# Optimization experiments

Hardware: AMD Instinct MI355X
Metric: run time of the kernel (lower is better)

Reference implementation:

```python
import jax, jax.numpy as jnp
import numpy as np
import math

N_EMBD = 1024
N_HEAD = 16
HEAD_DIM = N_EMBD // N_HEAD


def setup_inputs() -> dict:
    key = jax.random.key(0)
    k_x, k_w1, k_b1, k_w2, k_b2 = jax.random.split(key, 5)
    B, T = 2, 2048
    x = jax.random.normal(k_x, (B, T, N_EMBD), dtype=jnp.float32)
    # ln1: Linear(n_embd, 3*n_embd); weights stored as [in, out] for x @ W
    W_qkv = jax.random.normal(k_w1, (N_EMBD, 3 * N_EMBD), dtype=jnp.float32) * 0.02
    b_qkv = jax.random.normal(k_b1, (3 * N_EMBD,), dtype=jnp.float32) * 0.02
    # ln2: Linear(n_embd, n_embd)
    W_out = jax.random.normal(k_w2, (N_EMBD, N_EMBD), dtype=jnp.float32) * 0.02
    b_out = jax.random.normal(k_b2, (N_EMBD,), dtype=jnp.float32) * 0.02
    return {"x": x, "W_qkv": W_qkv, "b_qkv": b_qkv, "W_out": W_out, "b_out": b_out}


def reference(x, W_qkv, b_qkv, W_out, b_out):
    B, T, C = x.shape
    qkv = x @ W_qkv + b_qkv                      # [B,T,3C]
    q, k, v = jnp.split(qkv, 3, axis=-1)
    # reshape to heads: [B, H, T, D]
    def to_heads(t):
        return t.reshape(B, T, N_HEAD, HEAD_DIM).transpose(0, 2, 1, 3)
    Q, K, V = to_heads(q), to_heads(k), to_heads(v)
    # NOTE: scale is 1/sqrt(n_head), as in the source (not sqrt(head_dim));
    # NOTE: no causal mask is applied, faithfully matching the source forward.
    scale = 1.0 / math.sqrt(N_HEAD)
    scores = jnp.einsum('bhqd,bhkd->bhqk', Q, K) * scale  # [B,H,T,T]
    attn = jax.nn.softmax(scores, axis=-1)
    out = jnp.einsum('bhqk,bhkd->bhqd', attn, V)          # [B,H,T,D]
    out = out.transpose(0, 2, 1, 3).reshape(B, T, C)
    # dropout = 0.0 -> identity (eval mode)
    return out @ W_out + b_out
```

## Files before the change

kernel.cpp:

```cpp
#include <hip/hip_runtime.h>
#include <hip/hip_bf16.h>
#include <stdint.h>

typedef __bf16 bf16_t;
typedef __bf16 bf16x8 __attribute__((ext_vector_type(8)));
typedef float  f32x4  __attribute__((ext_vector_type(4)));

#define AS1 __attribute__((address_space(1)))
#define AS3 __attribute__((address_space(3)))

__device__ __forceinline__ void gload16(const bf16_t* g, char* l) {
  __builtin_amdgcn_global_load_lds((AS1 const void*)(uintptr_t)g, (AS3 void*)l, 16, 0, 0);
}
__device__ __forceinline__ int swz8(int r) { return (r & 7) ^ ((r >> 2) & 6); }

#define C2S 0.36067376022224085f
#define LGKM0 do { asm volatile("s_waitcnt lgkmcnt(0)" ::: "memory"); \
                   __builtin_amdgcn_sched_barrier(0); } while (0)

__global__ __launch_bounds__(256) void prep(
    const float* __restrict__ x, const float* __restrict__ Wqkv, const float* __restrict__ Wout,
    bf16_t* __restrict__ xb, bf16_t* __restrict__ wqkvT, bf16_t* __restrict__ woutT) {
  __shared__ float tile[32][33];
  const int bid = blockIdx.x, tid = threadIdx.x;
  if (bid < 4096) {
    const int i = bid * 256 + tid;
    float4 v = reinterpret_cast<const float4*>(x)[i];
    union { bf16_t h[4]; unsigned long long u; } r;
    r.h[0] = (bf16_t)v.x; r.h[1] = (bf16_t)v.y; r.h[2] = (bf16_t)v.z; r.h[3] = (bf16_t)v.w;
    reinterpret_cast<unsigned long long*>(xb)[i] = r.u;
    return;
  }
  const float* W; bf16_t* Wt; int N, tb;
  if (bid < 7168) { W = Wqkv; Wt = wqkvT; N = 3072; tb = bid - 4096; }
  else            { W = Wout; Wt = woutT; N = 1024; tb = bid - 7168; }
  const int kb = (tb & 31) * 32, nb = (tb >> 5) * 32;
  const int tx = tid & 31, ty = tid >> 5;
#pragma unroll
  for (int i = 0; i < 32; i += 8)
    tile[ty + i][tx] = W[(size_t)(kb + ty + i) * N + nb + tx];
  __syncthreads();
#pragma unroll
  for (int i = 0; i < 32; i += 8)
    Wt[(size_t)(nb + ty + i) * 1024 + kb + tx] = (bf16_t)tile[tx][ty + i];
}

template<int MI>
__global__ __launch_bounds__(256) void gemm_bt(
    const bf16_t* __restrict__ A, const bf16_t* __restrict__ Bt,
    const float* __restrict__ bias,
    bf16_t* __restrict__ outb, bf16_t* __restrict__ vtb, float* __restrict__ outf,
    int M, int N, int K, int ldo, int mode) {
  __shared__ bf16_t lA[3][MI * 1024];
  __shared__ bf16_t lB[3][4096];
  const int tid = threadIdx.x;
  const int wave = tid >> 6, lane = tid & 63;
  const int lr = lane & 15, lg = lane >> 4;
  const int ntiles = N >> 7;
  const int bid = (blockIdx.x & 7) * ((int)gridDim.x >> 3) + (blockIdx.x >> 3);
  const int bn = bid % ntiles, bm = bid / ntiles;
  const int m0 = bm * (MI * 32), n0 = bn * 128;
  const int wr = wave >> 1, wc = wave & 1;
  f32x4 acc[MI][4] = {};

  const int lamw = wave * 64 + lane;
  const int srow = lamw >> 2;
  const int scolb = ((lamw & 3) << 4) ^ (((srow >> 1) & 3) << 4);
  auto stageA = [&](int buf, int k0, int it) {
    gload16(A + (size_t)(m0 + it * 64 + srow) * K + k0 + (scolb >> 1),
            (char*)&lA[buf][0] + (it * 256 + wave * 64) * 16);
  };
  auto stageB = [&](int buf, int k0, int it) {
    gload16(Bt + (size_t)(n0 + it * 64 + srow) * K + k0 + (scolb >> 1),
            (char*)&lB[buf][0] + (it * 256 + wave * 64) * 16);
  };
  auto stageg = [&](int buf, int k0) {
#pragma unroll
    for (int it = 0; it < MI / 2; ++it) stageA(buf, k0, it);
    stageB(buf, k0, 0); stageB(buf, k0, 1);
  };

  auto ldA = [&](const char* p, int mi) {
    const int row = wr * (MI * 16) + mi * 16 + lr;
    return *reinterpret_cast<const bf16x8*>(p + row * 64 + ((lg * 16) ^ (((row >> 1) & 3) << 4)));
  };
  auto ldB = [&](const char* p, int ni) {
    const int row = wc * 64 + ni * 16 + lr;
    return *reinterpret_cast<const bf16x8*>(p + row * 64 + ((lg * 16) ^ (((row >> 1) & 3) << 4)));
  };

  const int nt = K >> 5;
  stageg(0, 0);
  stageg(1, 32);
  int cur = 0, stg = 2;

  for (int t = 0; t < nt; ++t) {
    if (t + 1 < nt) {
      if constexpr (MI == 4) asm volatile("s_waitcnt vmcnt(4)" ::: "memory");
      else                   asm volatile("s_waitcnt vmcnt(3)" ::: "memory");
    } else {
      asm volatile("s_waitcnt vmcnt(0)" ::: "memory");
    }
    __builtin_amdgcn_s_barrier();
    __builtin_amdgcn_sched_barrier(0);

    const char* pA = (const char*)&lA[cur][0];
    const char* pB = (const char*)&lB[cur][0];
    const bool pf = (t + 2 < nt);
    const int k2 = (t + 2) << 5;
    bf16x8 af[MI], bfv[4];

    if constexpr (MI == 4) {
      af[0] = ldA(pA, 0); af[1] = ldA(pA, 1);
      bfv[0] = ldB(pB, 0); bfv[1] = ldB(pB, 1);
      if (pf) stageA(stg, k2, 0);
      __builtin_amdgcn_s_barrier(); LGKM0;
      __builtin_amdgcn_s_setprio(1);
      acc[0][0] = __builtin_amdgcn_mfma_f32_16x16x32_bf16(af[0], bfv[0], acc[0][0], 0, 0, 0);
      acc[0][1] = __builtin_amdgcn_mfma_f32_16x16x32_bf16(af[0], bfv[1], acc[0][1], 0, 0, 0);
      acc[1][0] = __builtin_amdgcn_mfma_f32_16x16x32_bf16(af[1], bfv[0], acc[1][0], 0, 0, 0);
      acc[1][1] = __builtin_amdgcn_mfma_f32_16x16x32_bf16(af[1], bfv[1], acc[1][1], 0, 0, 0);
      __builtin_amdgcn_s_setprio(0);
      bfv[2] = ldB(pB, 2); bfv[3] = ldB(pB, 3);
      if (pf) stageA(stg, k2, 1);
      __builtin_amdgcn_s_barrier(); LGKM0;
      __builtin_amdgcn_s_setprio(1);
      acc[0][2] = __builtin_amdgcn_mfma_f32_16x16x32_bf16(af[0], bfv[2], acc[0][2], 0, 0, 0);
      acc[0][3] = __builtin_amdgcn_mfma_f32_16x16x32_bf16(af[0], bfv[3], acc[0][3], 0, 0, 0);
      acc[1][2] = __builtin_amdgcn_mfma_f32_16x16x32_bf16(af[1], bfv[2], acc[1][2], 0, 0, 0);
      acc[1][3] = __builtin_amdgcn_mfma_f32_16x16x32_bf16(af[1], bfv[3], acc[1][3], 0, 0, 0);
      __builtin_amdgcn_s_setprio(0);
      af[2] = ldA(pA, 2); af[3] = ldA(pA, 3);
      if (pf) stageB(stg, k2, 0);
      __builtin_amdgcn_s_barrier(); LGKM0;
      __builtin_amdgcn_s_setprio(1);
      acc[2][0] = __builtin_amdgcn_mfma_f32_16x16x32_bf16(af[2], bfv[0], acc[2][0], 0, 0, 0);
      acc[2][1] = __builtin_amdgcn_mfma_f32_16x16x32_bf16(af[2], bfv[1], acc[2][1], 0, 0, 0);
      acc[3][0] = __builtin_amdgcn_mfma_f32_16x16x32_bf16(af[3], bfv[0], acc[3][0], 0, 0, 0);
      acc[3][1] = __builtin_amdgcn_mfma_f32_16x16x32_bf16(af[3], bfv[1], acc[3][1], 0, 0, 0);
      __builtin_amdgcn_s_setprio(0);
      if (pf) stageB(stg, k2, 1);
      __builtin_amdgcn_s_barrier();
      __builtin_amdgcn_s_setprio(1);
      acc[2][2] = __builtin_amdgcn_mfma_f32_16x16x32_bf16(af[2], bfv[2], acc[2][2], 0, 0, 0);
      acc[2][3] = __builtin_amdgcn_mfma_f32_16x16x32_bf16(af[2], bfv[3], acc[2][3], 0, 0, 0);
      acc[3][2] = __builtin_amdgcn_mfma_f32_16x16x32_bf16(af[3], bfv[2], acc[3][2], 0, 0, 0);
      acc[3][3] = __builtin_amdgcn_mfma_f32_16x16x32_bf16(af[3], bfv[3], acc[3][3], 0, 0, 0);
      __builtin_amdgcn_s_setprio(0);
    } else {
      af[0] = ldA(pA, 0); af[1] = ldA(pA, 1);
      bfv[0] = ldB(pB, 0); bfv[1] = ldB(pB, 1);
      if (pf) { stageA(stg, k2, 0); stageB(stg, k2, 0); }
      __builtin_amdgcn_s_barrier(); LGKM0;
      __builtin_amdgcn_s_setprio(1);
      acc[0][0] = __builtin_amdgcn_mfma_f32_16x16x32_bf16(af[0], bfv[0], acc[0][0], 0, 0, 0);
      acc[0][1] = __builtin_amdgcn_mfma_f32_16x16x32_bf16(af[0], bfv[1], acc[0][1], 0, 0, 0);
      acc[1][0] = __builtin_amdgcn_mfma_f32_16x16x32_bf16(af[1], bfv[0], acc[1][0], 0, 0, 0);
      acc[1][1] = __builtin_amdgcn_mfma_f32_16x16x32_bf16(af[1], bfv[1], acc[1][1], 0, 0, 0);
      __builtin_amdgcn_s_setprio(0);
      bfv[2] = ldB(pB, 2); bfv[3] = ldB(pB, 3);
      if (pf) stageB(stg, k2, 1);
      __builtin_amdgcn_s_barrier(); LGKM0;
      __builtin_amdgcn_s_setprio(1);
      acc[0][2] = __builtin_amdgcn_mfma_f32_16x16x32_bf16(af[0], bfv[2], acc[0][2], 0, 0, 0);
      acc[0][3] = __builtin_amdgcn_mfma_f32_16x16x32_bf16(af[0], bfv[3], acc[0][3], 0, 0, 0);
      acc[1][2] = __builtin_amdgcn_mfma_f32_16x16x32_bf16(af[1], bfv[2], acc[1][2], 0, 0, 0);
      acc[1][3] = __builtin_amdgcn_mfma_f32_16x16x32_bf16(af[1], bfv[3], acc[1][3], 0, 0, 0);
      __builtin_amdgcn_s_setprio(0);
    }

    cur = cur == 2 ? 0 : cur + 1;
    stg = stg == 2 ? 0 : stg + 1;
  }

#pragma unroll
  for (int mi = 0; mi < MI; ++mi) {
#pragma unroll
    for (int ni = 0; ni < 4; ++ni) {
      const int col = n0 + wc * 64 + ni * 16 + lr;
      const float bv = bias[col];
      const int rg0 = m0 + wr * (MI * 16) + mi * 16 + lg * 4;
      if (mode == 1 && col >= 2048) {
        const int colv = col - 2048;
        const int dd = colv & 63, hh = colv >> 6;
        const int bb = rg0 >> 11, t = rg0 & 2047;
        union { bf16_t h4[4]; unsigned long long u; } pk;
#pragma unroll
        for (int r = 0; r < 4; ++r) pk.h4[r] = (bf16_t)(acc[mi][ni][r] + bv);
        *reinterpret_cast<unsigned long long*>(
            vtb + (size_t)(bb * 16 + hh) * 131072 + (size_t)dd * 2048 + t) = pk.u;
      } else {
        const float sc = (mode == 1 && col < 1024) ? C2S : 1.f;
#pragma unroll
        for (int r = 0; r < 4; ++r) {
          const float v = (acc[mi][ni][r] + bv) * sc;
          if (mode == 2) outf[(size_t)(rg0 + r) * ldo + col] = v;
          else           outb[(size_t)(rg0 + r) * ldo + col] = (bf16_t)v;
        }
      }
    }
  }
}

__global__ __launch_bounds__(512) void attn_fwd(
    const bf16_t* __restrict__ qkv2,
    const bf16_t* __restrict__ vT,
    bf16_t* __restrict__ a0, bf16_t* __restrict__ a1,
    float* __restrict__ lbuf) {
  __shared__ bf16_t lds[3][8192];
  const int tid = threadIdx.x;
  const int wave = tid >> 6, lane = tid & 63;
  const int lr = lane & 15, lg = lane >> 4;
  const int id = blockIdx.x;
  const int xcd = id & 7, slot = id >> 3;
  const int bh = xcd * 4 + (slot & 3);
  const int rest = slot >> 2;
  const int qb = rest & 7, kvh = rest >> 3;
  const int b = bh >> 4, h = bh & 15;

  const int q0 = qb * 256 + wave * 32;
  const bf16_t* Qp = qkv2 + (size_t)(b * 2048 + q0) * 2048 + h * 64;
  bf16x8 qf[2][2];
#pragma unroll
  for (int hx = 0; hx < 2; ++hx) {
    qf[hx][0] = *reinterpret_cast<const bf16x8*>(Qp + (size_t)(hx * 16 + lr) * 2048 + lg * 8);
    qf[hx][1] = *reinterpret_cast<const bf16x8*>(Qp + (size_t)(hx * 16 + lr) * 2048 + 32 + lg * 8);
  }

  const int kr = tid >> 3;
  const int ks = (tid & 7) ^ swz8(kr);
  const bf16_t* Ksrc = qkv2 + (size_t)(b * 2048 + kvh * 1024 + kr) * 2048 + 1024 + h * 64 + ks * 8;
  const bf16_t* Vsrc = vT + (size_t)bh * 131072 + (size_t)kr * 2048 + kvh * 1024 + ks * 8;

  auto stage = [&](int buf, int kb) {
    char* base = (char*)&lds[buf][0] + wave * 1024;
    gload16(Ksrc + (size_t)kb * 131072, base);
    gload16(Vsrc + (size_t)kb * 64, base + 8192);
  };

  int kofs[4][2], vofs[4][2];
#pragma unroll
  for (int t = 0; t < 4; ++t) {
    const int kk = 32 * (t >> 1) + 8 * (lr >> 2) + 4 * (t & 1) + (lr & 3);
    const int sw = swz8(kk) << 4;
    kofs[t][0] = (kk << 7) + ((lg * 16) ^ sw);
    kofs[t][1] = (kk << 7) + ((64 + lg * 16) ^ sw);
  }
#pragma unroll
  for (int nc = 0; nc < 4; ++nc) {
    const int vr = nc * 16 + lr;
    const int sw = swz8(vr) << 4;
    vofs[nc][0] = 8192 + (vr << 7) + ((lg * 16) ^ sw);
    vofs[nc][1] = 8192 + (vr << 7) + ((64 + lg * 16) ^ sw);
  }

  f32x4 acc[2][4] = {};
  f32x4 accl[2] = {};
  bf16x8 ones;
#pragma unroll
  for (int j = 0; j < 8; ++j) ones[j] = (bf16_t)1.0f;

  stage(0, 0);
  stage(1, 1);
  int cur = 0, stg = 2;

  for (int kb = 0; kb < 16; ++kb) {
    if (kb + 2 < 16) stage(stg, kb + 2);
    if (kb + 2 < 16)      asm volatile("s_waitcnt vmcnt(4)" ::: "memory");
    else if (kb + 1 < 16) asm volatile("s_waitcnt vmcnt(2)" ::: "memory");
    else                  asm volatile("s_waitcnt vmcnt(0)" ::: "memory");
    __builtin_amdgcn_s_barrier();
    __builtin_amdgcn_sched_barrier(0);
    const char* bK = (const char*)&lds[cur][0];

    f32x4 s[2][4];
#pragma unroll
    for (int t = 0; t < 4; ++t) {
      const bf16x8 k0 = *reinterpret_cast<const bf16x8*>(bK + kofs[t][0]);
      const bf16x8 k1 = *reinterpret_cast<const bf16x8*>(bK + kofs[t][1]);
#pragma unroll
      for (int hx = 0; hx < 2; ++hx) {
        f32x4 z = {0.f, 0.f, 0.f, 0.f};
        z = __builtin_amdgcn_mfma_f32_16x16x32_bf16(k0, qf[hx][0], z, 0, 0, 0);
        s[hx][t] = __builtin_amdgcn_mfma_f32_16x16x32_bf16(k1, qf[hx][1], z, 0, 0, 0);
      }
    }

    bf16x8 pa[2][2];
#pragma unroll
    for (int hx = 0; hx < 2; ++hx) {
      float p[16];
#pragma unroll
      for (int t = 0; t < 4; ++t)
#pragma unroll
        for (int r = 0; r < 4; ++r)
          p[t * 4 + r] = __builtin_amdgcn_exp2f(s[hx][t][r]);
#pragma unroll
      for (int j = 0; j < 8; ++j) { pa[hx][0][j] = (bf16_t)p[j]; pa[hx][1][j] = (bf16_t)p[8 + j]; }
    }

    __builtin_amdgcn_s_setprio(1);
#pragma unroll
    for (int hx = 0; hx < 2; ++hx) {
      accl[hx] = __builtin_amdgcn_mfma_f32_16x16x32_bf16(pa[hx][0], ones, accl[hx], 0, 0, 0);
      accl[hx] = __builtin_amdgcn_mfma_f32_16x16x32_bf16(pa[hx][1], ones, accl[hx], 0, 0, 0);
    }
#pragma unroll
    for (int nc = 0; nc < 4; ++nc) {
      const bf16x8 v0 = *reinterpret_cast<const bf16x8*>(bK + vofs[nc][0]);
      const bf16x8 v1 = *reinterpret_cast<const bf16x8*>(bK + vofs[nc][1]);
#pragma unroll
      for (int hx = 0; hx < 2; ++hx) {
        acc[hx][nc] = __builtin_amdgcn_mfma_f32_16x16x32_bf16(pa[hx][0], v0, acc[hx][nc], 0, 0, 0);
        acc[hx][nc] = __builtin_amdgcn_mfma_f32_16x16x32_bf16(pa[hx][1], v1, acc[hx][nc], 0, 0, 0);
      }
    }
    __builtin_amdgcn_s_setprio(0);

    __builtin_amdgcn_sched_barrier(0);
    __builtin_amdgcn_s_barrier();
    cur = cur == 2 ? 0 : cur + 1;
    stg = stg == 2 ? 0 : stg + 1;
  }

  bf16_t* ap = kvh ? a1 : a0;
#pragma unroll
  for (int hx = 0; hx < 2; ++hx) {
#pragma unroll
    for (int r = 0; r < 4; ++r) {
      const float lf = 1.f / accl[hx][r];
      const int qg = q0 + hx * 16 + lg * 4 + r;
      bf16_t* op = ap + (size_t)(b * 2048 + qg) * 1024 + h * 64 + lr;
#pragma unroll
      for (int nc = 0; nc < 4; ++nc) op[nc * 16] = (bf16_t)(acc[hx][nc][r] * lf);
      if (lr == 0)
        lbuf[(size_t)(kvh * 4096 + b * 2048 + qg) * 16 + h] = accl[hx][r];
    }
  }
}

__global__ void attn_reduce(const bf16_t* __restrict__ a0, const bf16_t* __restrict__ a1,
                            const float* __restrict__ lbuf, bf16_t* __restrict__ aout) {
  const int i = blockIdx.x * 256 + threadIdx.x;
  const int r = i >> 7, h = (i & 127) >> 3;
  const float l0 = lbuf[(size_t)r * 16 + h];
  const float l1 = lbuf[(size_t)(4096 + r) * 16 + h];
  const float inv = 1.f / (l0 + l1);
  const float w0 = l0 * inv, w1 = l1 * inv;
  const bf16x8 v0 = reinterpret_cast<const bf16x8*>(a0)[i];
  const bf16x8 v1 = reinterpret_cast<const bf16x8*>(a1)[i];
  bf16x8 o;
#pragma unroll
  for (int j = 0; j < 8; ++j) o[j] = (bf16_t)(w0 * (float)v0[j] + w1 * (float)v1[j]);
  reinterpret_cast<bf16x8*>(aout)[i] = o;
}

extern "C" void kernel_launch(void* const* d_in, const int* in_sizes, int n_in,
                              void* d_out, int out_size, void* d_ws, size_t ws_size,
                              hipStream_t stream) {
  (void)in_sizes; (void)n_in; (void)out_size; (void)ws_size;
  const float* x    = (const float*)d_in[0];
  const float* Wqkv = (const float*)d_in[1];
  const float* bqkv = (const float*)d_in[2];
  const float* Wout = (const float*)d_in[3];
  const float* bout = (const float*)d_in[4];
  float* out = (float*)d_out;

  char* ws = (char*)d_ws;
  bf16_t* xb    = (bf16_t*)(ws);
  bf16_t* a0    = (bf16_t*)(ws);
  bf16_t* wqkvT = (bf16_t*)(ws + 8388608);
  bf16_t* woutT = (bf16_t*)(ws + 14680064);
  bf16_t* qkv2  = (bf16_t*)(ws + 16777216);
  bf16_t* aout  = (bf16_t*)(ws + 16777216);
  bf16_t* vT    = (bf16_t*)(ws + 33554432);
  bf16_t* a1    = (bf16_t*)(ws + 41943040);
  float*  lbuf  = (float*)(ws + 50331648);

  prep<<<8192, 256, 0, stream>>>(x, Wqkv, Wout, xb, wqkvT, woutT);
  gemm_bt<4><<<768, 256, 0, stream>>>(xb, wqkvT, bqkv, qkv2, vT, nullptr, 4096, 3072, 1024, 2048, 1);
  attn_fwd<<<512, 512, 0, stream>>>(qkv2, vT, a0, a1, lbuf);
  attn_reduce<<<2048, 256, 0, stream>>>(a0, a1, lbuf, aout);
  gemm_bt<2><<<512, 256, 0, stream>>>(aout, woutT, bout, nullptr, nullptr, out, 4096, 1024, 1024, 1024, 2);
}
```

Baseline: 114.2 us.

## Use 8-wave 128x128 GEMM kernel for QKV projection with simpler pipeline

```diff
diff --git a/kernel.cpp b/kernel.cpp
--- a/kernel.cpp
+++ b/kernel.cpp
@@ -43,6 +43,109 @@
 #pragma unroll
   for (int i = 0; i < 32; i += 8)
     Wt[(size_t)(nb + ty + i) * 1024 + kb + tx] = (bf16_t)tile[tx][ty + i];
+}
+
+__global__ __launch_bounds__(512) void gemm8(
+    const bf16_t* __restrict__ A, const bf16_t* __restrict__ Bt,
+    const float* __restrict__ bias,
+    bf16_t* __restrict__ outb, bf16_t* __restrict__ vtb,
+    int N, int K, int ldo) {
+  __shared__ bf16_t lA[3][4096];
+  __shared__ bf16_t lB[3][4096];
+  const int tid = threadIdx.x;
+  const int wave = tid >> 6, lane = tid & 63;
+  const int lr = lane & 15, lg = lane >> 4;
+  const int ntiles = N >> 7;
+  const int bid = (blockIdx.x & 7) * ((int)gridDim.x >> 3) + (blockIdx.x >> 3);
+  const int bn = bid % ntiles, bm = bid / ntiles;
+  const int m0 = bm * 128, n0 = bn * 128;
+  const int wr = wave >> 2, wc = wave & 3;
+  f32x4 acc[4][2] = {};
+
+  const int srow = tid >> 2;
+  const int scolb = ((tid & 3) << 4) ^ (((srow >> 1) & 3) << 4);
+  const bf16_t* Asrc = A  + (size_t)(m0 + srow) * K + (scolb >> 1);
+  const bf16_t* Bsrc = Bt + (size_t)(n0 + srow) * K + (scolb >> 1);
+  auto stage = [&](int buf, int k0) {
+    char* dst = (char*)nullptr;
+    (void)dst;
+    gload16(Asrc + k0, (char*)&lA[buf][0] + wave * 1024);
+    gload16(Bsrc + k0, (char*)&lB[buf][0] + wave * 1024);
+  };
+
+  auto ldA = [&](const char* p, int mi) {
+    const int row = wr * 64 + mi * 16 + lr;
+    return *reinterpret_cast<const bf16x8*>(p + row * 64 + ((lg * 16) ^ (((row >> 1) & 3) << 4)));
+  };
+  auto ldB = [&](const char* p, int ni) {
+    const int row = wc * 32 + ni * 16 + lr;
+    return *reinterpret_cast<const bf16x8*>(p + row * 64 + ((lg * 16) ^ (((row >> 1) & 3) << 4)));
+  };
+
+  const int nt = K >> 5;
+  stage(0, 0);
+  stage(1, 32);
+  int cur = 0, stg = 2;
+
+  for (int t = 0; t < nt; ++t) {
+    if (t + 2 < nt) {
+      stage(stg, (t + 2) << 5);
+      asm volatile("s_waitcnt vmcnt(4)" ::: "memory");
+    } else if (t + 1 < nt) {
+      asm volatile("s_waitcnt vmcnt(2)" ::: "memory");
+    } else {
+      asm volatile("s_waitcnt vmcnt(0)" ::: "memory");
+    }
+    __builtin_amdgcn_s_barrier();
+    __builtin_amdgcn_sched_barrier(0);
+
+    const char* pA = (const char*)&lA[cur][0];
+    const char* pB = (const char*)&lB[cur][0];
+    bf16x8 af[4], bfv[2];
+#pragma unroll
+    for (int mi = 0; mi < 4; ++mi) af[mi] = ldA(pA, mi);
+    bfv[0] = ldB(pB, 0); bfv[1] = ldB(pB, 1);
+
+    __builtin_amdgcn_s_setprio(1);
+#pragma unroll
+    for (int mi = 0; mi < 4; ++mi)
+#pragma unroll
+      for (int ni = 0; ni < 2; ++ni)
+        acc[mi][ni] = __builtin_amdgcn_mfma_f32_16x16x32_bf16(af[mi], bfv[ni], acc[mi][ni], 0, 0, 0);
+    __builtin_amdgcn_s_setprio(0);
+
+    __builtin_amdgcn_sched_barrier(0);
+    __builtin_amdgcn_s_barrier();
+    cur = cur == 2 ? 0 : cur + 1;
+    stg = stg == 2 ? 0 : stg + 1;
+  }
+
+#pragma unroll
+  for (int mi = 0; mi < 4; ++mi) {
+#pragma unroll
+    for (int ni = 0; ni < 2; ++ni) {
+      const int col = n0 + wc * 32 + ni * 16 + lr;
+      const float bv = bias[col];
+      const int rg0 = m0 + wr * 64 + mi * 16 + lg * 4;
+      if (col >= 2048) {
+        const int colv = col - 2048;
+        const int dd = colv & 63, hh = colv >> 6;
+        const int bb = rg0 >> 11, t = rg0 & 2047;
+        union { bf16_t h4[4]; unsigned long long u; } pk;
+#pragma unroll
+        for (int r = 0; r < 4; ++r) pk.h4[r] = (bf16_t)(acc[mi][ni][r] + bv);
+        *reinterpret_cast<unsigned long long*>(
+            vtb + (size_t)(bb * 16 + hh) * 131072 + (size_t)dd * 2048 + t) = pk.u;
+      } else {
+        const float sc = (col < 1024) ? C2S : 1.f;
+#pragma unroll
+        for (int r = 0; r < 4; ++r) {
+          const float v = (acc[mi][ni][r] + bv) * sc;
+          outb[(size_t)(rg0 + r) * ldo + col] = (bf16_t)v;
+        }
+      }
+    }
+  }
 }
 
 template<int MI>
@@ -110,64 +213,25 @@
     const int k2 = (t + 2) << 5;
     bf16x8 af[MI], bfv[4];
 
-    if constexpr (MI == 4) {
-      af[0] = ldA(pA, 0); af[1] = ldA(pA, 1);
-      bfv[0] = ldB(pB, 0); bfv[1] = ldB(pB, 1);
-      if (pf) stageA(stg, k2, 0);
-      __builtin_amdgcn_s_barrier(); LGKM0;
-      __builtin_amdgcn_s_setprio(1);
-      acc[0][0] = __builtin_amdgcn_mfma_f32_16x16x32_bf16(af[0], bfv[0], acc[0][0], 0, 0, 0);
-      acc[0][1] = __builtin_amdgcn_mfma_f32_16x16x32_bf16(af[0], bfv[1], acc[0][1], 0, 0, 0);
-      acc[1][0] = __builtin_amdgcn_mfma_f32_16x16x32_bf16(af[1], bfv[0], acc[1][0], 0, 0, 0);
-      acc[1][1] = __builtin_amdgcn_mfma_f32_16x16x32_bf16(af[1], bfv[1], acc[1][1], 0, 0, 0);
-      __builtin_amdgcn_s_setprio(0);
-      bfv[2] = ldB(pB, 2); bfv[3] = ldB(pB, 3);
-      if (pf) stageA(stg, k2, 1);
-      __builtin_amdgcn_s_barrier(); LGKM0;
-      __builtin_amdgcn_s_setprio(1);
-      acc[0][2] = __builtin_amdgcn_mfma_f32_16x16x32_bf16(af[0], bfv[2], acc[0][2], 0, 0, 0);
-      acc[0][3] = __builtin_amdgcn_mfma_f32_16x16x32_bf16(af[0], bfv[3], acc[0][3], 0, 0, 0);
-      acc[1][2] = __builtin_amdgcn_mfma_f32_16x16x32_bf16(af[1], bfv[2], acc[1][2], 0, 0, 0);
-      acc[1][3] = __builtin_amdgcn_mfma_f32_16x16x32_bf16(af[1], bfv[3], acc[1][3], 0, 0, 0);
-      __builtin_amdgcn_s_setprio(0);
-      af[2] = ldA(pA, 2); af[3] = ldA(pA, 3);
-      if (pf) stageB(stg, k2, 0);
-      __builtin_amdgcn_s_barrier(); LGKM0;
-      __builtin_amdgcn_s_setprio(1);
-      acc[2][0] = __builtin_amdgcn_mfma_f32_16x16x32_bf16(af[2], bfv[0], acc[2][0], 0, 0, 0);
-      acc[2][1] = __builtin_amdgcn_mfma_f32_16x16x32_bf16(af[2], bfv[1], acc[2][1], 0, 0, 0);
-      acc[3][0] = __builtin_amdgcn_mfma_f32_16x16x32_bf16(af[3], bfv[0], acc[3][0], 0, 0, 0);
-      acc[3][1] = __builtin_amdgcn_mfma_f32_16x16x32_bf16(af[3], bfv[1], acc[3][1], 0, 0, 0);
-      __builtin_amdgcn_s_setprio(0);
-      if (pf) stageB(stg, k2, 1);
-      __builtin_amdgcn_s_barrier();
-      __builtin_amdgcn_s_setprio(1);
-      acc[2][2] = __builtin_amdgcn_mfma_f32_16x16x32_bf16(af[2], bfv[2], acc[2][2], 0, 0, 0);
-      acc[2][3] = __builtin_amdgcn_mfma_f32_16x16x32_bf16(af[2], bfv[3], acc[2][3], 0, 0, 0);
-      acc[3][2] = __builtin_amdgcn_mfma_f32_16x16x32_bf16(af[3], bfv[2], acc[3][2], 0, 0, 0);
-      acc[3][3] = __builtin_amdgcn_mfma_f32_16x16x32_bf16(af[3], bfv[3], acc[3][3], 0, 0, 0);
-      __builtin_amdgcn_s_setprio(0);
-    } else {
-      af[0] = ldA(pA, 0); af[1] = ldA(pA, 1);
-      bfv[0] = ldB(pB, 0); bfv[1] = ldB(pB, 1);
-      if (pf) { stageA(stg, k2, 0); stageB(stg, k2, 0); }
-      __builtin_amdgcn_s_barrier(); LGKM0;
-      __builtin_amdgcn_s_setprio(1);
-      acc[0][0] = __builtin_amdgcn_mfma_f32_16x16x32_bf16(af[0], bfv[0], acc[0][0], 0, 0, 0);
-      acc[0][1] = __builtin_amdgcn_mfma_f32_16x16x32_bf16(af[0], bfv[1], acc[0][1], 0, 0, 0);
-      acc[1][0] = __builtin_amdgcn_mfma_f32_16x16x32_bf16(af[1], bfv[0], acc[1][0], 0, 0, 0);
-      acc[1][1] = __builtin_amdgcn_mfma_f32_16x16x32_bf16(af[1], bfv[1], acc[1][1], 0, 0, 0);
-      __builtin_amdgcn_s_setprio(0);
-      bfv[2] = ldB(pB, 2); bfv[3] = ldB(pB, 3);
-      if (pf) stageB(stg, k2, 1);
-      __builtin_amdgcn_s_barrier(); LGKM0;
-      __builtin_amdgcn_s_setprio(1);
-      acc[0][2] = __builtin_amdgcn_mfma_f32_16x16x32_bf16(af[0], bfv[2], acc[0][2], 0, 0, 0);
-      acc[0][3] = __builtin_amdgcn_mfma_f32_16x16x32_bf16(af[0], bfv[3], acc[0][3], 0, 0, 0);
-      acc[1][2] = __builtin_amdgcn_mfma_f32_16x16x32_bf16(af[1], bfv[2], acc[1][2], 0, 0, 0);
-      acc[1][3] = __builtin_amdgcn_mfma_f32_16x16x32_bf16(af[1], bfv[3], acc[1][3], 0, 0, 0);
-      __builtin_amdgcn_s_setprio(0);
-    }
+    af[0] = ldA(pA, 0); af[1] = ldA(pA, 1);
+    bfv[0] = ldB(pB, 0); bfv[1] = ldB(pB, 1);
+    if (pf) { stageA(stg, k2, 0); stageB(stg, k2, 0); }
+    __builtin_amdgcn_s_barrier(); LGKM0;
+    __builtin_amdgcn_s_setprio(1);
+    acc[0][0] = __builtin_amdgcn_mfma_f32_16x16x32_bf16(af[0], bfv[0], acc[0][0], 0, 0, 0);
+    acc[0][1] = __builtin_amdgcn_mfma_f32_16x16x32_bf16(af[0], bfv[1], acc[0][1], 0, 0, 0);
+    acc[1][0] = __builtin_amdgcn_mfma_f32_16x16x32_bf16(af[1], bfv[0], acc[1][0], 0, 0, 0);
+    acc[1][1] = __builtin_amdgcn_mfma_f32_16x16x32_bf16(af[1], bfv[1], acc[1][1], 0, 0, 0);
+    __builtin_amdgcn_s_setprio(0);
+    bfv[2] = ldB(pB, 2); bfv[3] = ldB(pB, 3);
+    if (pf) stageB(stg, k2, 1);
+    __builtin_amdgcn_s_barrier(); LGKM0;
+    __builtin_amdgcn_s_setprio(1);
+    acc[0][2] = __builtin_amdgcn_mfma_f32_16x16x32_bf16(af[0], bfv[2], acc[0][2], 0, 0, 0);
+    acc[0][3] = __builtin_amdgcn_mfma_f32_16x16x32_bf16(af[0], bfv[3], acc[0][3], 0, 0, 0);
+    acc[1][2] = __builtin_amdgcn_mfma_f32_16x16x32_bf16(af[1], bfv[2], acc[1][2], 0, 0, 0);
+    acc[1][3] = __builtin_amdgcn_mfma_f32_16x16x32_bf16(af[1], bfv[3], acc[1][3], 0, 0, 0);
+    __builtin_amdgcn_s_setprio(0);
 
     cur = cur == 2 ? 0 : cur + 1;
     stg = stg == 2 ? 0 : stg + 1;
@@ -180,26 +244,16 @@
       const int col = n0 + wc * 64 + ni * 16 + lr;
       const float bv = bias[col];
       const int rg0 = m0 + wr * (MI * 16) + mi * 16 + lg * 4;
-      if (mode == 1 && col >= 2048) {
-        const int colv = col - 2048;
-        const int dd = colv & 63, hh = colv >> 6;
-        const int bb = rg0 >> 11, t = rg0 & 2047;
-        union { bf16_t h4[4]; unsigned long long u; } pk;
-#pragma unroll
-        for (int r = 0; r < 4; ++r) pk.h4[r] = (bf16_t)(acc[mi][ni][r] + bv);
-        *reinterpret_cast<unsigned long long*>(
-            vtb + (size_t)(bb * 16 + hh) * 131072 + (size_t)dd * 2048 + t) = pk.u;
-      } else {
-        const float sc = (mode == 1 && col < 1024) ? C2S : 1.f;
-#pragma unroll
-        for (int r = 0; r < 4; ++r) {
-          const float v = (acc[mi][ni][r] + bv) * sc;
-          if (mode == 2) outf[(size_t)(rg0 + r) * ldo + col] = v;
-          else           outb[(size_t)(rg0 + r) * ldo + col] = (bf16_t)v;
-        }
+      const float sc = 1.f;
+#pragma unroll
+      for (int r = 0; r < 4; ++r) {
+        const float v = (acc[mi][ni][r] + bv) * sc;
+        if (mode == 2) outf[(size_t)(rg0 + r) * ldo + col] = v;
+        else           outb[(size_t)(rg0 + r) * ldo + col] = (bf16_t)v;
       }
     }
   }
+  (void)vtb;
 }
 
 __global__ __launch_bounds__(512) void attn_fwd(
@@ -378,7 +432,7 @@
   float*  lbuf  = (float*)(ws + 50331648);
 
   prep<<<8192, 256, 0, stream>>>(x, Wqkv, Wout, xb, wqkvT, woutT);
-  gemm_bt<4><<<768, 256, 0, stream>>>(xb, wqkvT, bqkv, qkv2, vT, nullptr, 4096, 3072, 1024, 2048, 1);
+  gemm8<<<768, 512, 0, stream>>>(xb, wqkvT, bqkv, qkv2, vT, 3072, 1024, 2048);
   attn_fwd<<<512, 512, 0, stream>>>(qkv2, vT, a0, a1, lbuf);
   attn_reduce<<<2048, 256, 0, stream>>>(a0, a1, lbuf, aout);
   gemm_bt<2><<<512, 256, 0, stream>>>(aout, woutT, bout, nullptr, nullptr, out, 4096, 1024, 1024, 1024, 2);
```

After: 111.6 us. -2.3%, faster.
